# Performance work log

Hardware: AMD Instinct MI355X
Metric: run time of the kernel (lower is better)

Reference implementation:

```python
import jax, jax.numpy as jnp
import numpy as np

TEMP = 0.1
COEFF = 0.5
WARMUP = 0
S = 32 * 32  # hardcoded in the torch module


def _l2n(x, axis):
    # matches F.normalize(p=2, eps=1e-12)
    n = jnp.linalg.norm(x, axis=axis, keepdims=True)
    return x / jnp.maximum(n, 1e-12)


def _ce_first_class(pos, neg):
    # cross-entropy with label 0 on logits = [pos | neg] / T
    logits = jnp.concatenate([pos, neg], axis=1) / TEMP
    return jnp.mean(jax.nn.logsumexp(logits, axis=1) - logits[:, 0])


def _dense_losses(q_of, q_x, k_of, k_x, k_avg_dense):
    # q_of,k_of: (B,d,S) normalized; q_x,k_x: (B,C,S) normalized; k_avg_dense: (B,C) UN-normalized (torch bug preserved)
    B, C, _ = q_x.shape
    sim = jnp.einsum('bds,bdt->bst', q_of, k_of)          # (B,S,S)
    ind = jnp.argmax(sim, axis=2)                          # (B,S)
    idxg = jnp.take_along_axis(k_x, jnp.broadcast_to(ind[:, None, :], k_x.shape), axis=2)
    idxg = jax.lax.stop_gradient(idxg)                     # computed under torch.no_grad
    l_pos = jnp.sum(q_x * idxg, axis=1).reshape(-1, 1)     # (B*S,1)
    qf = jnp.transpose(q_x, (0, 2, 1)).reshape(-1, C)      # (B*S,C)
    l_neg_full = qf @ k_avg_dense.T                        # (B*S,B)
    # static mask: row n excludes column n // S
    base = np.stack([np.delete(np.arange(B), i) for i in range(B)])  # (B,B-1)
    neg_cols = jnp.asarray(np.repeat(base, S, axis=0))     # (B*S,B-1)
    l_neg = jnp.take_along_axis(l_neg_full, neg_cols, axis=1)
    return l_pos, l_neg


def _forward(original_features_q, avgpooled_global_q, x_q, avgpooled_dense_q,
             original_features_k, avgpooled_global_k, x_k, avgpooled_dense_k, epoch):
    of = jnp.concatenate([original_features_q, original_features_k], axis=0)
    ag = jnp.concatenate([avgpooled_global_q, avgpooled_global_k], axis=0)
    x = jnp.concatenate([x_q, x_k], axis=0)
    ad = jnp.concatenate([avgpooled_dense_q, avgpooled_dense_k], axis=0)

    # global InfoNCE
    agn = _l2n(ag, 1)
    sim = agn @ agn.T                                      # (2B,2B)
    n2 = sim.shape[0]
    B = n2 // 2
    rows = np.arange(n2)
    pos_cols = (rows + B) % n2
    pos = sim[jnp.asarray(rows), jnp.asarray(pos_cols)][:, None]
    neg_cols = np.stack([np.setdiff1d(rows, [i, pos_cols[i]]) for i in range(n2)])  # (2B,2B-2)
    neg = jnp.take_along_axis(sim, jnp.asarray(neg_cols), axis=1)
    global_loss = _ce_first_class(pos, neg)

    # dense InfoNCE
    b, d, h, w = of.shape
    of = _l2n(of.reshape(b, d, h * w), 1)
    xn = _l2n(x, 1)
    q_of, k_of = of[:b // 2], of[b // 2:]
    q_x, k_x = xn[:b // 2], xn[b // 2:]
    q_ad, k_ad = ad[:b // 2], ad[b // 2:]  # NOTE: un-normalized, matching the torch code
    p1, n1 = _dense_losses(q_of, q_x, k_of, k_x, k_ad)
    p2, n2_ = _dense_losses(k_of, k_x, q_of, q_x, q_ad)
    dense_loss = _ce_first_class(jnp.concatenate([p1, p2], axis=0),
                                 jnp.concatenate([n1, n2_], axis=0))

    if epoch > WARMUP:
        return COEFF * global_loss + (1.0 - COEFF) * dense_loss
    return global_loss


def setup_inputs() -> dict:
    key = jax.random.key(0)
    ks = jax.random.split(key, 8)
    B, d, C, h, w = 64, 256, 128, 32, 32
    return {
        'original_features_q': jax.random.normal(ks[0], (B, d, h, w), jnp.float32),
        'avgpooled_global_q': jax.random.normal(ks[1], (B, C), jnp.float32),
        'x_q': jax.random.normal(ks[2], (B, C, h * w), jnp.float32),
        'avgpooled_dense_q': jax.random.normal(ks[3], (B, C), jnp.float32),
        'original_features_k': jax.random.normal(ks[4], (B, d, h, w), jnp.float32),
        'avgpooled_global_k': jax.random.normal(ks[5], (B, C), jnp.float32),
        'x_k': jax.random.normal(ks[6], (B, C, h * w), jnp.float32),
        'avgpooled_dense_k': jax.random.normal(ks[7], (B, C), jnp.float32),
        'epoch': 5,
    }


def reference(original_features_q, avgpooled_global_q, x_q, avgpooled_dense_q,
              original_features_k, avgpooled_global_k, x_k, avgpooled_dense_k, epoch):
    return _forward(original_features_q, avgpooled_global_q, x_q, avgpooled_dense_q,
                    original_features_k, avgpooled_global_k, x_k, avgpooled_dense_k, epoch)
```

## Files before the change

kernel.cpp:

```cpp
#include <hip/hip_runtime.h>
#include <math.h>

#define TEMP_INV 10.0f

typedef unsigned long long u64;
typedef __attribute__((ext_vector_type(8))) __bf16 bf16x8;
typedef __attribute__((ext_vector_type(4))) float f32x4;

__device__ inline unsigned fkey(float v) {
  unsigned u = __float_as_uint(v);
  return (u & 0x80000000u) ? ~u : (u | 0x80000000u);
}
__device__ inline u64 packvi(float v, unsigned idx) {
  return ((u64)fkey(v) << 32) | (u64)(0xFFFFFFFFu - idx);
}

__device__ __forceinline__ void async_copy16(const void* gp, void* lp) {
  __builtin_amdgcn_global_load_lds(
      (__attribute__((address_space(1))) void*)(unsigned long long)gp,
      (__attribute__((address_space(3))) void*)(unsigned long long)lp,
      16, 0, 0);
}

__global__ __launch_bounds__(256) void kcvt(const float* __restrict__ ofq,
                                            const float* __restrict__ ofk,
                                            __bf16* __restrict__ ofT,
                                            float* __restrict__ of_invn) {
  int s0 = blockIdx.x * 32, b = blockIdx.y;
  const float* src = (b < 64) ? (ofq + (size_t)b * 262144) : (ofk + (size_t)(b - 64) * 262144);
  __shared__ __bf16 T[32][36];
  __shared__ float R[8][32];
  int t = threadIdx.x;
  int dd = t >> 5, ss = t & 31;
  int wr = t >> 3, wd = t & 7;
  float ssq = 0.f;
  __bf16* out = ofT + (size_t)b * 262144 + (size_t)s0 * 256;
  for (int d0 = 0; d0 < 256; d0 += 32) {
    float v[4];
#pragma unroll
    for (int it = 0; it < 4; ++it) {
      int d = d0 + dd + 8 * it;
      v[it] = src[(size_t)d * 1024 + s0 + ss];
      ssq += v[it] * v[it];
    }
    __syncthreads();
#pragma unroll
    for (int it = 0; it < 4; ++it) T[ss][dd + 8 * it] = (__bf16)v[it];
    __syncthreads();
    *(uint2*)(out + (size_t)wr * 256 + d0 + wd * 4) = *(const uint2*)(&T[wr][wd * 4]);
  }
  R[dd][ss] = ssq;
  __syncthreads();
  if (t < 32) {
    float a = 0.f;
#pragma unroll
    for (int r = 0; r < 8; ++r) a += R[r][t];
    of_invn[b * 1024 + s0 + t] = 1.0f / fmaxf(sqrtf(a), 1e-12f);
  }
}

__global__ void kprep(const float* __restrict__ xq, const float* __restrict__ xk,
                      float* __restrict__ x_invn,
                      const float* __restrict__ adq, const float* __restrict__ adk,
                      float* __restrict__ adt) {
  if (blockIdx.x < 512) {
    int idx = blockIdx.x * 256 + threadIdx.x;
    int b = idx >> 10, s = idx & 1023;
    const float* src = (b < 64) ? (xq + (size_t)b * 131072) : (xk + (size_t)(b - 64) * 131072);
    float acc = 0.f;
#pragma unroll 8
    for (int c = 0; c < 128; ++c) { float v = src[c * 1024 + s]; acc += v * v; }
    x_invn[idx] = 1.0f / fmaxf(sqrtf(acc), 1e-12f);
  } else {
    int i = (blockIdx.x - 512) * 256 + threadIdx.x;
    int dir = i >> 13, r = i & 8191;
    int j = r >> 7, c = r & 127;
    const float* ad = dir == 0 ? adk : adq;
    adt[dir * 8192 + c * 64 + j] = ad[j * 128 + c];
  }
}

__global__ __launch_bounds__(256) void ksim(
    const __bf16* __restrict__ ofT, const float* __restrict__ of_invn,
    u64* __restrict__ best_row, u64* __restrict__ best_col) {
  int b = blockIdx.z;
  int s0 = blockIdx.x * 128, t0 = blockIdx.y * 128;
  const __bf16* Ag = ofT + (size_t)b * 262144;
  const __bf16* Bg = ofT + (size_t)(b + 64) * 262144;
  __shared__ __bf16 As[2][4096];
  __shared__ __bf16 Bs[2][4096];
  __shared__ float siq[128], sik[128];
  int t = threadIdx.x;
  if (t < 128) siq[t] = of_invn[b * 1024 + s0 + t];
  else sik[t - 128] = of_invn[65536 + b * 1024 + t0 + (t - 128)];

  f32x4 acc[4][4];
#pragma unroll
  for (int i = 0; i < 4; ++i)
#pragma unroll
    for (int j = 0; j < 4; ++j) acc[i][j] = (f32x4)(0.f);

  int lane = t & 63, w = t >> 6;
  int lc = lane & 15, q = lane >> 4;
  int wm = w & 1, wn = w >> 1;

  int aoff[4], boff[4];
#pragma unroll
  for (int i = 0; i < 4; ++i) {
    int mr = wm * 64 + i * 16 + lc;
    aoff[i] = mr * 32 + (((q + mr + (mr >> 2)) & 3) << 3);
    int nc = wn * 64 + i * 16 + lc;
    boff[i] = nc * 32 + (((q + nc + (nc >> 2)) & 3) << 3);
  }

  int kp = t & 3;
  int mA0 = t >> 2, lgA0 = (kp - mA0 - (mA0 >> 2)) & 3;
  int mA1 = 64 + (t >> 2), lgA1 = (kp - mA1 - (mA1 >> 2)) & 3;

  async_copy16(Ag + (size_t)(s0 + mA0) * 256 + lgA0 * 8, (char*)&As[0][0] + t * 16);
  async_copy16(Bg + (size_t)(t0 + mA0) * 256 + lgA0 * 8, (char*)&Bs[0][0] + t * 16);
  async_copy16(Ag + (size_t)(s0 + mA1) * 256 + lgA1 * 8, (char*)&As[0][0] + 4096 + t * 16);
  async_copy16(Bg + (size_t)(t0 + mA1) * 256 + lgA1 * 8, (char*)&Bs[0][0] + 4096 + t * 16);
  __syncthreads();

  for (int it = 0; it < 8; ++it) {
    int buf = it & 1;
    bf16x8 af[4], bfr[4];
#pragma unroll
    for (int i = 0; i < 4; ++i) af[i] = *(const bf16x8*)(&As[buf][0] + aoff[i]);
#pragma unroll
    for (int j = 0; j < 4; ++j) bfr[j] = *(const bf16x8*)(&Bs[buf][0] + boff[j]);
    if (it < 7) {
      int k0 = (it + 1) * 32;
      async_copy16(Ag + (size_t)(s0 + mA0) * 256 + k0 + lgA0 * 8, (char*)&As[buf ^ 1][0] + t * 16);
      async_copy16(Bg + (size_t)(t0 + mA0) * 256 + k0 + lgA0 * 8, (char*)&Bs[buf ^ 1][0] + t * 16);
      async_copy16(Ag + (size_t)(s0 + mA1) * 256 + k0 + lgA1 * 8, (char*)&As[buf ^ 1][0] + 4096 + t * 16);
      async_copy16(Bg + (size_t)(t0 + mA1) * 256 + k0 + lgA1 * 8, (char*)&Bs[buf ^ 1][0] + 4096 + t * 16);
    }
#pragma unroll
    for (int i = 0; i < 4; ++i)
#pragma unroll
      for (int j = 0; j < 4; ++j)
        acc[i][j] = __builtin_amdgcn_mfma_f32_16x16x32_bf16(af[i], bfr[j], acc[i][j], 0, 0, 0);
    __syncthreads();
  }

  float sk[4], sq[16];
#pragma unroll
  for (int j = 0; j < 4; ++j) sk[j] = sik[wn * 64 + j * 16 + lc];
#pragma unroll
  for (int i = 0; i < 4; ++i)
#pragma unroll
    for (int e = 0; e < 4; ++e) sq[i * 4 + e] = siq[wm * 64 + i * 16 + q * 4 + e];

  u64* browb = best_row + (size_t)b * 1024 + s0;
  u64* bcolb = best_col + (size_t)b * 1024 + t0;

#pragma unroll
  for (int i = 0; i < 4; ++i) {
#pragma unroll
    for (int e = 0; e < 4; ++e) {
      float v[4];
#pragma unroll
      for (int j = 0; j < 4; ++j) v[j] = acc[i][j][e] * sk[j];
      float vb = fmaxf(fmaxf(v[0], v[1]), fmaxf(v[2], v[3]));
#pragma unroll
      for (int mask = 1; mask <= 8; mask <<= 1) vb = fmaxf(vb, __shfl_xor(vb, mask));
      unsigned ib = 0xFFFFFFFFu;
#pragma unroll
      for (int j = 0; j < 4; ++j) {
        unsigned cand = (v[j] == vb) ? (unsigned)(t0 + wn * 64 + j * 16 + lc) : 0xFFFFFFFFu;
        ib = min(ib, cand);
      }
#pragma unroll
      for (int mask = 1; mask <= 8; mask <<= 1) ib = min(ib, __shfl_xor(ib, mask));
      if (lc == 0)
        atomicMax(browb + wm * 64 + i * 16 + q * 4 + e, ((u64)fkey(vb) << 32) | (u64)(0xFFFFFFFFu - ib));
    }
  }

#pragma unroll
  for (int j = 0; j < 4; ++j) {
    float cb = -INFINITY;
#pragma unroll
    for (int i = 0; i < 4; ++i)
#pragma unroll
      for (int e = 0; e < 4; ++e) cb = fmaxf(cb, acc[i][j][e] * sq[i * 4 + e]);
    cb = fmaxf(cb, __shfl_xor(cb, 16));
    cb = fmaxf(cb, __shfl_xor(cb, 32));
    unsigned ib = 0xFFFFFFFFu;
#pragma unroll
    for (int i = 0; i < 4; ++i)
#pragma unroll
      for (int e = 0; e < 4; ++e) {
        float m2 = acc[i][j][e] * sq[i * 4 + e];
        unsigned cand = (m2 == cb) ? (unsigned)(s0 + wm * 64 + i * 16 + q * 4 + e) : 0xFFFFFFFFu;
        ib = min(ib, cand);
      }
    ib = min(ib, __shfl_xor(ib, 16));
    ib = min(ib, __shfl_xor(ib, 32));
    if (lane < 16)
      atomicMax(bcolb + wn * 64 + j * 16 + lane, ((u64)fkey(cb) << 32) | (u64)(0xFFFFFFFFu - ib));
  }
}

__global__ __launch_bounds__(1024) void kpos(
    const float* __restrict__ xq, const float* __restrict__ xk,
    const float* __restrict__ x_invn,
    const u64* __restrict__ best_row, const u64* __restrict__ best_col,
    float* __restrict__ posl) {
  int b = blockIdx.x, dir = blockIdx.y;
  const float* xsrc = dir == 0 ? xq : xk;
  const float* xdst = dir == 0 ? xk : xq;
  const float* inv_src = x_invn + (dir ? 65536 : 0);
  const float* inv_dst = x_invn + (dir ? 0 : 65536);
  const u64* best = dir == 0 ? best_row : best_col;

  __shared__ float xrow[8][1024];
  __shared__ float sdinv[1024];
  int t = threadIdx.x;
  sdinv[t] = inv_dst[b * 1024 + t];
  u64 p = best[(size_t)b * 1024 + t];
  int sidx = (int)(0xFFFFFFFFu - (unsigned)(p & 0xFFFFFFFFull));
  const float* xsb = xsrc + (size_t)b * 131072;
  const float* xdb = xdst + (size_t)b * 131072;
  float acc = 0.f;
  for (int c0 = 0; c0 < 128; c0 += 8) {
    __syncthreads();
#pragma unroll
    for (int qq = 0; qq < 2; ++qq)
      ((float4*)xrow)[t + 1024 * qq] = ((const float4*)(xdb + (size_t)c0 * 1024))[t + 1024 * qq];
    __syncthreads();
#pragma unroll
    for (int cc = 0; cc < 8; ++cc)
      acc += xsb[(size_t)(c0 + cc) * 1024 + t] * xrow[cc][sidx];
  }
  posl[dir * 65536 + b * 1024 + t] = acc * inv_src[b * 1024 + t] * sdinv[sidx] * TEMP_INV;
}

__global__ __launch_bounds__(256) void kneg(
    const float* __restrict__ xq, const float* __restrict__ xk,
    const float* __restrict__ x_invn,
    const float* __restrict__ adt, const float* __restrict__ posl,
    float* __restrict__ dsum) {
  int st = blockIdx.x, b = blockIdx.y, dir = blockIdx.z;
  const float* xsrc = dir == 0 ? xq : xk;
  const float* inv_src = x_invn + (dir ? 65536 : 0);
  const float* Bt = adt + dir * 8192;

  __shared__ float As2[64][64];
  __shared__ float Bs2[128][64];
  __shared__ float red[16];

  int tid = threadIdx.x;
  int tx = tid & 15, ty = tid >> 4;
  int s0 = st * 64;

#pragma unroll
  for (int qq = 0; qq < 8; ++qq)
    reinterpret_cast<float4*>(Bs2)[tid + 256 * qq] =
        reinterpret_cast<const float4*>(Bt)[tid + 256 * qq];

  float acc[4][4];
#pragma unroll
  for (int i = 0; i < 4; ++i)
#pragma unroll
    for (int j = 0; j < 4; ++j) acc[i][j] = 0.f;

  int lm = tid & 63, lk = tid >> 6;
  float sinv = inv_src[b * 1024 + s0 + lm];
  const float* xb = xsrc + (size_t)b * 131072;

  for (int k0 = 0; k0 < 128; k0 += 64) {
#pragma unroll
    for (int r = 0; r < 16; ++r) {
      int kk = lk + 4 * r;
      As2[kk][lm] = xb[(k0 + kk) * 1024 + s0 + lm] * sinv;
    }
    __syncthreads();
#pragma unroll
    for (int kk = 0; kk < 64; ++kk) {
      float4 av = *reinterpret_cast<const float4*>(&As2[kk][ty * 4]);
      float4 bv = *reinterpret_cast<const float4*>(&Bs2[k0 + kk][tx * 4]);
      float a[4] = {av.x, av.y, av.z, av.w};
      float bb[4] = {bv.x, bv.y, bv.z, bv.w};
#pragma unroll
      for (int i = 0; i < 4; ++i)
#pragma unroll
        for (int j = 0; j < 4; ++j) acc[i][j] += a[i] * bb[j];
    }
    __syncthreads();
  }

  float lsum = 0.f;
#pragma unroll
  for (int i = 0; i < 4; ++i) {
    int s = s0 + ty * 4 + i;
    float pos = posl[dir * 65536 + b * 1024 + s];
    float lg[4];
    float mloc = -INFINITY;
#pragma unroll
    for (int j = 0; j < 4; ++j) {
      int jg = tx * 4 + j;
      lg[j] = (jg == b) ? -INFINITY : acc[i][j] * TEMP_INV;
      mloc = fmaxf(mloc, lg[j]);
    }
#pragma unroll
    for (int mask = 1; mask <= 8; mask <<= 1) mloc = fmaxf(mloc, __shfl_xor(mloc, mask));
    float m = fmaxf(mloc, pos);
    float e = 0.f;
#pragma unroll
    for (int j = 0; j < 4; ++j) e += __expf(lg[j] - m);
#pragma unroll
    for (int mask = 1; mask <= 8; mask <<= 1) e += __shfl_xor(e, mask);
    if (tx == 0) lsum += m + __logf(e + __expf(pos - m)) - pos;
  }
  if (tx == 0) red[ty] = lsum;
  __syncthreads();
  if (tid == 0) {
    float v = 0.f;
#pragma unroll
    for (int r = 0; r < 16; ++r) v += red[r];
    atomicAdd(dsum, v);
  }
}

__global__ void kglobal(const float* __restrict__ agq, const float* __restrict__ agk,
                        float* __restrict__ gsum) {
  __shared__ float logits[128];
  __shared__ float rinv[128];
  int i = blockIdx.x, j = threadIdx.x;
  const float* rowi = (i < 64) ? (agq + i * 128) : (agk + (i - 64) * 128);
  const float* rowj = (j < 64) ? (agq + j * 128) : (agk + (j - 64) * 128);
  float dot = 0.f, nj = 0.f;
#pragma unroll 8
  for (int c = 0; c < 128; ++c) { float a = rowi[c], bb = rowj[c]; dot += a * bb; nj += bb * bb; }
  rinv[j] = 1.0f / fmaxf(sqrtf(nj), 1e-12f);
  __syncthreads();
  logits[j] = dot * rinv[i] * rinv[j] * TEMP_INV;
  __syncthreads();
  if (j == 0) {
    int pos = (i + 64) & 127;
    float m = -INFINITY;
    for (int t = 0; t < 128; ++t) if (t != i) m = fmaxf(m, logits[t]);
    float e = 0.f;
    for (int t = 0; t < 128; ++t) if (t != i) e += __expf(logits[t] - m);
    atomicAdd(gsum, m + __logf(e) - logits[pos]);
  }
}

__global__ void kfinal(const float* __restrict__ gsum, const float* __restrict__ dsum,
                       const int* __restrict__ epoch, float* __restrict__ out) {
  if (threadIdx.x == 0) {
    float g = gsum[0] / 128.0f;
    float dn = dsum[0] / 131072.0f;
    out[0] = (epoch[0] > 0) ? (0.5f * g + 0.5f * dn) : g;
  }
}

extern "C" void kernel_launch(void* const* d_in, const int* in_sizes, int n_in,
                              void* d_out, int out_size, void* d_ws, size_t ws_size,
                              hipStream_t stream) {
  const float* ofq = (const float*)d_in[0];
  const float* agq = (const float*)d_in[1];
  const float* xq  = (const float*)d_in[2];
  const float* adq = (const float*)d_in[3];
  const float* ofk = (const float*)d_in[4];
  const float* agk = (const float*)d_in[5];
  const float* xk  = (const float*)d_in[6];
  const float* adk = (const float*)d_in[7];
  const int* epoch = (const int*)d_in[8];
  float* out = (float*)d_out;

  char* wsb = (char*)d_ws;
  __bf16* ofT = (__bf16*)wsb;
  u64* best_row = (u64*)(wsb + 67108864);
  u64* best_col = best_row + 65536;
  float* gsum = (float*)(best_col + 65536);
  float* dsum = gsum + 1;
  float* posl = dsum + 1;
  float* x_invn  = posl + 131072;
  float* of_invn = x_invn + 131072;
  float* adt = of_invn + 131072;

  hipMemsetAsync(best_row, 0, 65536ull * 8 * 2 + 8, stream);

  dim3 gc(32, 128);
  kcvt<<<gc, 256, 0, stream>>>(ofq, ofk, ofT, of_invn);
  kprep<<<576, 256, 0, stream>>>(xq, xk, x_invn, adq, adk, adt);
  kglobal<<<128, 128, 0, stream>>>(agq, agk, gsum);

  dim3 gs(8, 8, 64);
  ksim<<<gs, 256, 0, stream>>>(ofT, of_invn, best_row, best_col);

  dim3 gp(64, 2);
  kpos<<<gp, 1024, 0, stream>>>(xq, xk, x_invn, best_row, best_col, posl);

  dim3 gn(16, 64, 2);
  kneg<<<gn, 256, 0, stream>>>(xq, xk, x_invn, adt, posl, dsum);

  kfinal<<<1, 1, 0, stream>>>(gsum, dsum, epoch, out);
}
```

Measured before the change: 422.4 us.

## Convert x to transposed bf16, use MFMA for negatives, drop LDS staging in ksim

Adds a kernel that transposes x into a bf16 (B,S,C) buffer stored over the dead ofT workspace, and fuses norm computation into it. kpos becomes a per-element gather dot product over contiguous bf16 rows, and kneg switches from an FP32 SIMT GEMM to bf16 MFMA. ksim drops LDS double buffering and loads MFMA fragments straight from global memory with register prefetch. These cut memory traffic and FP32 ALU work in exchange for bf16 rounding in the positive and negative logits, plus less data reuse in ksim.

```diff
diff --git a/kernel.cpp b/kernel.cpp
--- a/kernel.cpp
+++ b/kernel.cpp
@@ -11,16 +11,8 @@
   unsigned u = __float_as_uint(v);
   return (u & 0x80000000u) ? ~u : (u | 0x80000000u);
 }
-__device__ inline u64 packvi(float v, unsigned idx) {
-  return ((u64)fkey(v) << 32) | (u64)(0xFFFFFFFFu - idx);
-}
-
-__device__ __forceinline__ void async_copy16(const void* gp, void* lp) {
-  __builtin_amdgcn_global_load_lds(
-      (__attribute__((address_space(1))) void*)(unsigned long long)gp,
-      (__attribute__((address_space(3))) void*)(unsigned long long)lp,
-      16, 0, 0);
-}
+__device__ inline float bl16(unsigned u) { return __uint_as_float(u << 16); }
+__device__ inline float bh16(unsigned u) { return __uint_as_float(u & 0xFFFF0000u); }
 
 __global__ __launch_bounds__(256) void kcvt(const float* __restrict__ ofq,
                                             const float* __restrict__ ofk,
@@ -59,24 +51,51 @@
   }
 }
 
-__global__ void kprep(const float* __restrict__ xq, const float* __restrict__ xk,
-                      float* __restrict__ x_invn,
-                      const float* __restrict__ adq, const float* __restrict__ adk,
-                      float* __restrict__ adt) {
-  if (blockIdx.x < 512) {
-    int idx = blockIdx.x * 256 + threadIdx.x;
-    int b = idx >> 10, s = idx & 1023;
-    const float* src = (b < 64) ? (xq + (size_t)b * 131072) : (xk + (size_t)(b - 64) * 131072);
-    float acc = 0.f;
-#pragma unroll 8
-    for (int c = 0; c < 128; ++c) { float v = src[c * 1024 + s]; acc += v * v; }
-    x_invn[idx] = 1.0f / fmaxf(sqrtf(acc), 1e-12f);
-  } else {
-    int i = (blockIdx.x - 512) * 256 + threadIdx.x;
-    int dir = i >> 13, r = i & 8191;
-    int j = r >> 7, c = r & 127;
-    const float* ad = dir == 0 ? adk : adq;
-    adt[dir * 8192 + c * 64 + j] = ad[j * 128 + c];
+__global__ __launch_bounds__(256) void kcvt_x(const float* __restrict__ xq,
+                                              const float* __restrict__ xk,
+                                              __bf16* __restrict__ xT,
+                                              float* __restrict__ x_invn,
+                                              const float* __restrict__ adq,
+                                              const float* __restrict__ adk,
+                                              __bf16* __restrict__ ad16) {
+  int y = blockIdx.y, t = threadIdx.x;
+  if (y == 128) {
+    int i = blockIdx.x * 512 + t * 2;
+    const float* src = (i < 8192) ? adk : adq;
+    int r = i & 8191;
+    ad16[i] = (__bf16)src[r];
+    ad16[i + 1] = (__bf16)src[r + 1];
+    return;
+  }
+  int s0 = blockIdx.x * 32, b = y;
+  const float* src = (b < 64) ? (xq + (size_t)b * 131072) : (xk + (size_t)(b - 64) * 131072);
+  __shared__ __bf16 T[32][36];
+  __shared__ float R[8][32];
+  int dd = t >> 5, ss = t & 31;
+  int wr = t >> 3, wd = t & 7;
+  float ssq = 0.f;
+  __bf16* out = xT + (size_t)b * 131072 + (size_t)s0 * 128;
+  for (int d0 = 0; d0 < 128; d0 += 32) {
+    float v[4];
+#pragma unroll
+    for (int it = 0; it < 4; ++it) {
+      int d = d0 + dd + 8 * it;
+      v[it] = src[(size_t)d * 1024 + s0 + ss];
+      ssq += v[it] * v[it];
+    }
+    __syncthreads();
+#pragma unroll
+    for (int it = 0; it < 4; ++it) T[ss][dd + 8 * it] = (__bf16)v[it];
+    __syncthreads();
+    *(uint2*)(out + (size_t)wr * 128 + d0 + wd * 4) = *(const uint2*)(&T[wr][wd * 4]);
+  }
+  R[dd][ss] = ssq;
+  __syncthreads();
+  if (t < 32) {
+    float a = 0.f;
+#pragma unroll
+    for (int r = 0; r < 8; ++r) a += R[r][t];
+    x_invn[b * 1024 + s0 + t] = 1.0f / fmaxf(sqrtf(a), 1e-12f);
   }
 }
 
@@ -85,73 +104,54 @@
     u64* __restrict__ best_row, u64* __restrict__ best_col) {
   int b = blockIdx.z;
   int s0 = blockIdx.x * 128, t0 = blockIdx.y * 128;
-  const __bf16* Ag = ofT + (size_t)b * 262144;
-  const __bf16* Bg = ofT + (size_t)(b + 64) * 262144;
-  __shared__ __bf16 As[2][4096];
-  __shared__ __bf16 Bs[2][4096];
-  __shared__ float siq[128], sik[128];
-  int t = threadIdx.x;
-  if (t < 128) siq[t] = of_invn[b * 1024 + s0 + t];
-  else sik[t - 128] = of_invn[65536 + b * 1024 + t0 + (t - 128)];
-
-  f32x4 acc[4][4];
-#pragma unroll
-  for (int i = 0; i < 4; ++i)
-#pragma unroll
-    for (int j = 0; j < 4; ++j) acc[i][j] = (f32x4)(0.f);
-
-  int lane = t & 63, w = t >> 6;
+  int t = threadIdx.x, lane = t & 63, w = t >> 6;
   int lc = lane & 15, q = lane >> 4;
   int wm = w & 1, wn = w >> 1;
 
-  int aoff[4], boff[4];
+  const __bf16* Ab = ofT + (size_t)b * 262144 + (size_t)(s0 + wm * 64) * 256 + q * 8;
+  const __bf16* Bb = ofT + (size_t)(b + 64) * 262144 + (size_t)(t0 + wn * 64) * 256 + q * 8;
+
+  f32x4 acc[4][4];
+#pragma unroll
+  for (int i = 0; i < 4; ++i)
+#pragma unroll
+    for (int j = 0; j < 4; ++j) acc[i][j] = (f32x4)(0.f);
+
+  bf16x8 ac[4], bc[4], an[4], bn[4];
 #pragma unroll
   for (int i = 0; i < 4; ++i) {
-    int mr = wm * 64 + i * 16 + lc;
-    aoff[i] = mr * 32 + (((q + mr + (mr >> 2)) & 3) << 3);
-    int nc = wn * 64 + i * 16 + lc;
-    boff[i] = nc * 32 + (((q + nc + (nc >> 2)) & 3) << 3);
-  }
-
-  int kp = t & 3;
-  int mA0 = t >> 2, lgA0 = (kp - mA0 - (mA0 >> 2)) & 3;
-  int mA1 = 64 + (t >> 2), lgA1 = (kp - mA1 - (mA1 >> 2)) & 3;
-
-  async_copy16(Ag + (size_t)(s0 + mA0) * 256 + lgA0 * 8, (char*)&As[0][0] + t * 16);
-  async_copy16(Bg + (size_t)(t0 + mA0) * 256 + lgA0 * 8, (char*)&Bs[0][0] + t * 16);
-  async_copy16(Ag + (size_t)(s0 + mA1) * 256 + lgA1 * 8, (char*)&As[0][0] + 4096 + t * 16);
-  async_copy16(Bg + (size_t)(t0 + mA1) * 256 + lgA1 * 8, (char*)&Bs[0][0] + 4096 + t * 16);
-  __syncthreads();
-
+    ac[i] = *(const bf16x8*)(Ab + (i * 16 + lc) * 256);
+    bc[i] = *(const bf16x8*)(Bb + (i * 16 + lc) * 256);
+  }
+#pragma unroll
   for (int it = 0; it < 8; ++it) {
-    int buf = it & 1;
-    bf16x8 af[4], bfr[4];
-#pragma unroll
-    for (int i = 0; i < 4; ++i) af[i] = *(const bf16x8*)(&As[buf][0] + aoff[i]);
-#pragma unroll
-    for (int j = 0; j < 4; ++j) bfr[j] = *(const bf16x8*)(&Bs[buf][0] + boff[j]);
     if (it < 7) {
       int k0 = (it + 1) * 32;
-      async_copy16(Ag + (size_t)(s0 + mA0) * 256 + k0 + lgA0 * 8, (char*)&As[buf ^ 1][0] + t * 16);
-      async_copy16(Bg + (size_t)(t0 + mA0) * 256 + k0 + lgA0 * 8, (char*)&Bs[buf ^ 1][0] + t * 16);
-      async_copy16(Ag + (size_t)(s0 + mA1) * 256 + k0 + lgA1 * 8, (char*)&As[buf ^ 1][0] + 4096 + t * 16);
-      async_copy16(Bg + (size_t)(t0 + mA1) * 256 + k0 + lgA1 * 8, (char*)&Bs[buf ^ 1][0] + 4096 + t * 16);
+#pragma unroll
+      for (int i = 0; i < 4; ++i) {
+        an[i] = *(const bf16x8*)(Ab + (i * 16 + lc) * 256 + k0);
+        bn[i] = *(const bf16x8*)(Bb + (i * 16 + lc) * 256 + k0);
+      }
     }
 #pragma unroll
     for (int i = 0; i < 4; ++i)
 #pragma unroll
       for (int j = 0; j < 4; ++j)
-        acc[i][j] = __builtin_amdgcn_mfma_f32_16x16x32_bf16(af[i], bfr[j], acc[i][j], 0, 0, 0);
-    __syncthreads();
+        acc[i][j] = __builtin_amdgcn_mfma_f32_16x16x32_bf16(ac[i], bc[j], acc[i][j], 0, 0, 0);
+    if (it < 7) {
+#pragma unroll
+      for (int i = 0; i < 4; ++i) { ac[i] = an[i]; bc[i] = bn[i]; }
+    }
   }
 
   float sk[4], sq[16];
 #pragma unroll
-  for (int j = 0; j < 4; ++j) sk[j] = sik[wn * 64 + j * 16 + lc];
+  for (int j = 0; j < 4; ++j) sk[j] = of_invn[65536 + b * 1024 + t0 + wn * 64 + j * 16 + lc];
 #pragma unroll
   for (int i = 0; i < 4; ++i)
 #pragma unroll
-    for (int e = 0; e < 4; ++e) sq[i * 4 + e] = siq[wm * 64 + i * 16 + q * 4 + e];
+    for (int e = 0; e < 4; ++e)
+      sq[i * 4 + e] = of_invn[b * 1024 + s0 + wm * 64 + i * 16 + q * 4 + e];
 
   u64* browb = best_row + (size_t)b * 1024 + s0;
   u64* bcolb = best_col + (size_t)b * 1024 + t0;
@@ -175,10 +175,10 @@
 #pragma unroll
       for (int mask = 1; mask <= 8; mask <<= 1) ib = min(ib, __shfl_xor(ib, mask));
       if (lc == 0)
-        atomicMax(browb + wm * 64 + i * 16 + q * 4 + e, ((u64)fkey(vb) << 32) | (u64)(0xFFFFFFFFu - ib));
-    }
-  }
-
+        atomicMax(browb + wm * 64 + i * 16 + q * 4 + e,
+                  ((u64)fkey(vb) << 32) | (u64)(0xFFFFFFFFu - ib));
+    }
+  }
 #pragma unroll
   for (int j = 0; j < 4; ++j) {
     float cb = -INFINITY;
@@ -200,129 +200,105 @@
     ib = min(ib, __shfl_xor(ib, 16));
     ib = min(ib, __shfl_xor(ib, 32));
     if (lane < 16)
-      atomicMax(bcolb + wn * 64 + j * 16 + lane, ((u64)fkey(cb) << 32) | (u64)(0xFFFFFFFFu - ib));
-  }
-}
-
-__global__ __launch_bounds__(1024) void kpos(
-    const float* __restrict__ xq, const float* __restrict__ xk,
-    const float* __restrict__ x_invn,
+      atomicMax(bcolb + wn * 64 + j * 16 + lane,
+                ((u64)fkey(cb) << 32) | (u64)(0xFFFFFFFFu - ib));
+  }
+}
+
+__global__ __launch_bounds__(256) void kpos(
+    const __bf16* __restrict__ xT, const float* __restrict__ x_invn,
     const u64* __restrict__ best_row, const u64* __restrict__ best_col,
     float* __restrict__ posl) {
-  int b = blockIdx.x, dir = blockIdx.y;
-  const float* xsrc = dir == 0 ? xq : xk;
-  const float* xdst = dir == 0 ? xk : xq;
-  const float* inv_src = x_invn + (dir ? 65536 : 0);
-  const float* inv_dst = x_invn + (dir ? 0 : 65536);
-  const u64* best = dir == 0 ? best_row : best_col;
-
-  __shared__ float xrow[8][1024];
-  __shared__ float sdinv[1024];
-  int t = threadIdx.x;
-  sdinv[t] = inv_dst[b * 1024 + t];
-  u64 p = best[(size_t)b * 1024 + t];
-  int sidx = (int)(0xFFFFFFFFu - (unsigned)(p & 0xFFFFFFFFull));
-  const float* xsb = xsrc + (size_t)b * 131072;
-  const float* xdb = xdst + (size_t)b * 131072;
+  int idx = blockIdx.x * 256 + threadIdx.x;
+  int dir = idx >> 16, r = idx & 65535;
+  int b = r >> 10, s = r & 1023;
+  const u64* best = dir ? best_col : best_row;
+  u64 p = best[r];
+  int ind = (int)(0xFFFFFFFFu - (unsigned)(p & 0xFFFFFFFFull));
+  int srcb = dir ? 64 + b : b, dstb = dir ? b : 64 + b;
+  const uint4* rs = (const uint4*)(xT + (size_t)srcb * 131072 + (size_t)s * 128);
+  const uint4* rd = (const uint4*)(xT + (size_t)dstb * 131072 + (size_t)ind * 128);
   float acc = 0.f;
-  for (int c0 = 0; c0 < 128; c0 += 8) {
-    __syncthreads();
-#pragma unroll
-    for (int qq = 0; qq < 2; ++qq)
-      ((float4*)xrow)[t + 1024 * qq] = ((const float4*)(xdb + (size_t)c0 * 1024))[t + 1024 * qq];
-    __syncthreads();
-#pragma unroll
-    for (int cc = 0; cc < 8; ++cc)
-      acc += xsb[(size_t)(c0 + cc) * 1024 + t] * xrow[cc][sidx];
-  }
-  posl[dir * 65536 + b * 1024 + t] = acc * inv_src[b * 1024 + t] * sdinv[sidx] * TEMP_INV;
+#pragma unroll
+  for (int i = 0; i < 8; ++i) {
+    uint4 a = rs[i], d = rd[i];
+    acc += bl16(a.x) * bl16(d.x) + bh16(a.x) * bh16(d.x);
+    acc += bl16(a.y) * bl16(d.y) + bh16(a.y) * bh16(d.y);
+    acc += bl16(a.z) * bl16(d.z) + bh16(a.z) * bh16(d.z);
+    acc += bl16(a.w) * bl16(d.w) + bh16(a.w) * bh16(d.w);
+  }
+  float invs = x_invn[(dir ? 65536 : 0) + r];
+  float invd = x_invn[(dir ? 0 : 65536) + b * 1024 + ind];
+  posl[idx] = acc * invs * invd * TEMP_INV;
 }
 
 __global__ __launch_bounds__(256) void kneg(
-    const float* __restrict__ xq, const float* __restrict__ xk,
-    const float* __restrict__ x_invn,
-    const float* __restrict__ adt, const float* __restrict__ posl,
+    const __bf16* __restrict__ xT, const float* __restrict__ x_invn,
+    const __bf16* __restrict__ ad16, const float* __restrict__ posl,
     float* __restrict__ dsum) {
   int st = blockIdx.x, b = blockIdx.y, dir = blockIdx.z;
-  const float* xsrc = dir == 0 ? xq : xk;
-  const float* inv_src = x_invn + (dir ? 65536 : 0);
-  const float* Bt = adt + dir * 8192;
-
-  __shared__ float As2[64][64];
-  __shared__ float Bs2[128][64];
-  __shared__ float red[16];
-
-  int tid = threadIdx.x;
-  int tx = tid & 15, ty = tid >> 4;
-  int s0 = st * 64;
-
-#pragma unroll
-  for (int qq = 0; qq < 8; ++qq)
-    reinterpret_cast<float4*>(Bs2)[tid + 256 * qq] =
-        reinterpret_cast<const float4*>(Bt)[tid + 256 * qq];
-
-  float acc[4][4];
+  int t = threadIdx.x, lane = t & 63, w = t >> 6;
+  int lc = lane & 15, q = lane >> 4;
+  int sbase = st * 256 + w * 64;
+
+  const __bf16* Ab = xT + (size_t)(dir * 64 + b) * 131072 + (size_t)sbase * 128 + q * 8;
+  const __bf16* Bb = ad16 + dir * 8192 + q * 8;
+  const float* invs = x_invn + (dir ? 65536 : 0) + b * 1024;
+  const float* posb = posl + dir * 65536 + b * 1024;
+
+  f32x4 acc[4][4];
 #pragma unroll
   for (int i = 0; i < 4; ++i)
 #pragma unroll
-    for (int j = 0; j < 4; ++j) acc[i][j] = 0.f;
-
-  int lm = tid & 63, lk = tid >> 6;
-  float sinv = inv_src[b * 1024 + s0 + lm];
-  const float* xb = xsrc + (size_t)b * 131072;
-
-  for (int k0 = 0; k0 < 128; k0 += 64) {
-#pragma unroll
-    for (int r = 0; r < 16; ++r) {
-      int kk = lk + 4 * r;
-      As2[kk][lm] = xb[(k0 + kk) * 1024 + s0 + lm] * sinv;
-    }
-    __syncthreads();
-#pragma unroll
-    for (int kk = 0; kk < 64; ++kk) {
-      float4 av = *reinterpret_cast<const float4*>(&As2[kk][ty * 4]);
-      float4 bv = *reinterpret_cast<const float4*>(&Bs2[k0 + kk][tx * 4]);
-      float a[4] = {av.x, av.y, av.z, av.w};
-      float bb[4] = {bv.x, bv.y, bv.z, bv.w};
-#pragma unroll
-      for (int i = 0; i < 4; ++i)
-#pragma unroll
-        for (int j = 0; j < 4; ++j) acc[i][j] += a[i] * bb[j];
-    }
-    __syncthreads();
+    for (int j = 0; j < 4; ++j) acc[i][j] = (f32x4)(0.f);
+
+#pragma unroll
+  for (int k = 0; k < 4; ++k) {
+    bf16x8 af[4], bfr[4];
+#pragma unroll
+    for (int i = 0; i < 4; ++i) af[i] = *(const bf16x8*)(Ab + (i * 16 + lc) * 128 + k * 32);
+#pragma unroll
+    for (int j = 0; j < 4; ++j) bfr[j] = *(const bf16x8*)(Bb + (j * 16 + lc) * 128 + k * 32);
+#pragma unroll
+    for (int i = 0; i < 4; ++i)
+#pragma unroll
+      for (int j = 0; j < 4; ++j)
+        acc[i][j] = __builtin_amdgcn_mfma_f32_16x16x32_bf16(af[i], bfr[j], acc[i][j], 0, 0, 0);
   }
 
   float lsum = 0.f;
 #pragma unroll
   for (int i = 0; i < 4; ++i) {
-    int s = s0 + ty * 4 + i;
-    float pos = posl[dir * 65536 + b * 1024 + s];
-    float lg[4];
-    float mloc = -INFINITY;
-#pragma unroll
-    for (int j = 0; j < 4; ++j) {
-      int jg = tx * 4 + j;
-      lg[j] = (jg == b) ? -INFINITY : acc[i][j] * TEMP_INV;
-      mloc = fmaxf(mloc, lg[j]);
-    }
-#pragma unroll
-    for (int mask = 1; mask <= 8; mask <<= 1) mloc = fmaxf(mloc, __shfl_xor(mloc, mask));
-    float m = fmaxf(mloc, pos);
-    float e = 0.f;
-#pragma unroll
-    for (int j = 0; j < 4; ++j) e += __expf(lg[j] - m);
-#pragma unroll
-    for (int mask = 1; mask <= 8; mask <<= 1) e += __shfl_xor(e, mask);
-    if (tx == 0) lsum += m + __logf(e + __expf(pos - m)) - pos;
-  }
-  if (tx == 0) red[ty] = lsum;
-  __syncthreads();
-  if (tid == 0) {
-    float v = 0.f;
-#pragma unroll
-    for (int r = 0; r < 16; ++r) v += red[r];
-    atomicAdd(dsum, v);
-  }
+#pragma unroll
+    for (int e = 0; e < 4; ++e) {
+      int s = sbase + i * 16 + q * 4 + e;
+      float sinv = invs[s];
+      float lg[4];
+      float mloc = -INFINITY;
+#pragma unroll
+      for (int jf = 0; jf < 4; ++jf) {
+        int jg = jf * 16 + lc;
+        lg[jf] = (jg == b) ? -INFINITY : acc[i][jf][e] * sinv * TEMP_INV;
+        mloc = fmaxf(mloc, lg[jf]);
+      }
+#pragma unroll
+      for (int mask = 1; mask <= 8; mask <<= 1) mloc = fmaxf(mloc, __shfl_xor(mloc, mask));
+      float pos = posb[s];
+      float m = fmaxf(mloc, pos);
+      float es = 0.f;
+#pragma unroll
+      for (int jf = 0; jf < 4; ++jf) es += __expf(lg[jf] - m);
+#pragma unroll
+      for (int mask = 1; mask <= 8; mask <<= 1) es += __shfl_xor(es, mask);
+      if (lc == 0) lsum += m + __logf(es + __expf(pos - m)) - pos;
+    }
+  }
+  lsum += __shfl_xor(lsum, 16);
+  lsum += __shfl_xor(lsum, 32);
+  __shared__ float wred[4];
+  if (lane == 0) wred[w] = lsum;
+  __syncthreads();
+  if (t == 0) atomicAdd(dsum, wred[0] + wred[1] + wred[2] + wred[3]);
 }
 
 __global__ void kglobal(const float* __restrict__ agq, const float* __restrict__ agk,
@@ -374,30 +350,33 @@
 
   char* wsb = (char*)d_ws;
   __bf16* ofT = (__bf16*)wsb;
+  __bf16* xT  = (__bf16*)wsb;
   u64* best_row = (u64*)(wsb + 67108864);
   u64* best_col = best_row + 65536;
-  float* gsum = (float*)(best_col + 65536);
+  float* posl = (float*)(best_col + 65536);
+  float* x_invn = posl + 131072;
+  float* of_invn = x_invn + 131072;
+  __bf16* ad16 = (__bf16*)(of_invn + 131072);
+  float* gsum = (float*)(ad16 + 16384);
   float* dsum = gsum + 1;
-  float* posl = dsum + 1;
-  float* x_invn  = posl + 131072;
-  float* of_invn = x_invn + 131072;
-  float* adt = of_invn + 131072;
-
-  hipMemsetAsync(best_row, 0, 65536ull * 8 * 2 + 8, stream);
+
+  hipMemsetAsync(best_row, 0, 65536ull * 8 * 2, stream);
+  hipMemsetAsync(gsum, 0, 8, stream);
 
   dim3 gc(32, 128);
   kcvt<<<gc, 256, 0, stream>>>(ofq, ofk, ofT, of_invn);
-  kprep<<<576, 256, 0, stream>>>(xq, xk, x_invn, adq, adk, adt);
   kglobal<<<128, 128, 0, stream>>>(agq, agk, gsum);
 
   dim3 gs(8, 8, 64);
   ksim<<<gs, 256, 0, stream>>>(ofT, of_invn, best_row, best_col);
 
-  dim3 gp(64, 2);
-  kpos<<<gp, 1024, 0, stream>>>(xq, xk, x_invn, best_row, best_col, posl);
-
-  dim3 gn(16, 64, 2);
-  kneg<<<gn, 256, 0, stream>>>(xq, xk, x_invn, adt, posl, dsum);
+  dim3 gx(32, 129);
+  kcvt_x<<<gx, 256, 0, stream>>>(xq, xk, xT, x_invn, adq, adk, ad16);
+
+  kpos<<<512, 256, 0, stream>>>(xT, x_invn, best_row, best_col, posl);
+
+  dim3 gn(4, 64, 2);
+  kneg<<<gn, 256, 0, stream>>>(xT, x_invn, ad16, posl, dsum);
 
   kfinal<<<1, 1, 0, stream>>>(gsum, dsum, epoch, out);
 }
```

Result: slower. 463.9 us (+9.8%).
